# Kernel tuning notes

Hardware: AMD Instinct MI355X
Metric: run time of the kernel (lower is better)

Reference implementation:

```python
import jax, jax.numpy as jnp
import numpy as np

T, B, I, H = 512, 64, 512, 512


def setup_inputs() -> dict:
    key = jax.random.key(0)
    ks = jax.random.split(key, 24)
    s = (1.0 / H) ** 0.5  # uniform_(-sqrt(1/hidden), sqrt(1/hidden))
    u = lambda k, shape: jax.random.uniform(k, shape, jnp.float32, -s, s)
    inp = {
        "x": jax.random.normal(ks[0], (T, B, I), jnp.float32),
        "h0": u(ks[1], (B, H)),
        "c0": u(ks[2], (B, H)),
    }
    j = 3
    for g in ("ii", "if", "ig", "io"):
        inp["W_" + g] = u(ks[j], (I, H)); j += 1
        inp["b_" + g] = u(ks[j], (H,)); j += 1
    for g in ("hi", "hf", "hg", "ho"):
        inp["W_" + g] = u(ks[j], (H, H)); j += 1
        inp["b_" + g] = u(ks[j], (H,)); j += 1
    return inp


def reference(x, h0, c0, W_ii, b_ii, W_if, b_if, W_ig, b_ig, W_io, b_io,
              W_hi, b_hi, W_hf, b_hf, W_hg, b_hg, W_ho, b_ho):
    # Concatenating per-gate weights is mathematically identical to the 8
    # separate matmuls + bias adds in the source cell.
    Wx = jnp.concatenate([W_ii, W_if, W_ig, W_io], axis=1)        # [I, 4H]
    Wh = jnp.concatenate([W_hi, W_hf, W_hg, W_ho], axis=1)        # [H, 4H]
    b = jnp.concatenate([b_ii + b_hi, b_if + b_hf, b_ig + b_hg, b_io + b_ho])
    # Precompute all input projections in one big GEMM: [T, B, 4H]
    xg = jnp.einsum('tbi,ih->tbh', x, Wx) + b

    def step(carry, xg_t):
        h, c = carry
        gates = xg_t + h @ Wh                                      # [B, 4H]
        i_g, f_g, g_g, o_g = jnp.split(gates, 4, axis=-1)
        i = jax.nn.sigmoid(i_g)
        f = jax.nn.sigmoid(f_g)
        g = jnp.tanh(g_g)
        o = jax.nn.sigmoid(o_g)
        c1 = f * c + i * g
        h1 = o * c1  # NOTE: source applies o * c_1 WITHOUT tanh(c_1)
        return (h1, c1), h1

    (hT, cT), out = jax.lax.scan(step, (h0, c0), xg)               # out: [T, B, H]
    return (out, hT, cT)
```

## Files before the change

kernel.cpp:

```cpp
#include <hip/hip_runtime.h>
#include <stdint.h>


typedef __attribute__((ext_vector_type(8))) short    short8;
typedef __attribute__((ext_vector_type(4))) float    f32x4;
typedef __attribute__((ext_vector_type(4))) unsigned u32x4;
typedef __attribute__((ext_vector_type(2))) unsigned u32x2;

#define XG_OFF    0ull
#define WBT_OFF   134217728ull
#define BIAS_OFF  136314880ull
#define HW_OFF    136323072ull

static __device__ __forceinline__ unsigned short f2bf(float f) {
  unsigned u = __float_as_uint(f);
  unsigned r = (u + 0x7FFFu + ((u >> 16) & 1u)) >> 16;
  return (unsigned short)r;
}
static __device__ __forceinline__ float bf2f(unsigned short u) {
  return __uint_as_float(((unsigned)u) << 16);
}
static __device__ __forceinline__ float sigmoidf_(float x) {
  return 1.0f / (1.0f + __expf(-x));
}
static __device__ __forceinline__ float tanhf_(float x) {
  return 1.0f - 2.0f / (__expf(2.0f * x) + 1.0f);
}

__global__ void lstm_prep(const float* __restrict__ W_ii, const float* __restrict__ W_if,
                          const float* __restrict__ W_ig, const float* __restrict__ W_io,
                          const float* __restrict__ b_ii, const float* __restrict__ b_if,
                          const float* __restrict__ b_ig, const float* __restrict__ b_io,
                          const float* __restrict__ b_hi, const float* __restrict__ b_hf,
                          const float* __restrict__ b_hg, const float* __restrict__ b_ho,
                          const float* __restrict__ h0, unsigned char* ws)
{
  unsigned short*     WbT  = (unsigned short*)(ws + WBT_OFF);
  float*              bias = (float*)(ws + BIAS_OFF);
  unsigned long long* hw64 = (unsigned long long*)(ws + HW_OFF);

  const int gid = blockIdx.x * blockDim.x + threadIdx.x;
  const int gsz = gridDim.x * blockDim.x;

  for (int i = gid; i < 4 * 512 * 512; i += gsz) {
    int g = i >> 18, rem = i & 262143, c = rem >> 9, k = rem & 511;
    const float* W = (g == 0) ? W_ii : (g == 1) ? W_if : (g == 2) ? W_ig : W_io;
    WbT[(size_t)(g * 512 + c) * 512 + k] = f2bf(W[(size_t)k * 512 + c]);
  }
  for (int i = gid; i < 2048; i += gsz) {
    int g = i >> 9, c = i & 511;
    const float* bi = (g == 0) ? b_ii : (g == 1) ? b_if : (g == 2) ? b_ig : b_io;
    const float* bh = (g == 0) ? b_hi : (g == 1) ? b_hf : (g == 2) ? b_hg : b_ho;
    bias[i] = bi[c] + bh[c];
  }
  for (int i = gid; i < 64 * 256; i += gsz) {
    int r = i >> 8, wc = i & 255;
    int gb = r >> 4, row = r & 15, wsl = wc >> 6, c = wc & 63;
    unsigned lo = f2bf(h0[(size_t)r * 512 + wc * 2]);
    unsigned hi = f2bf(h0[(size_t)r * 512 + wc * 2 + 1]);
    hw64[((size_t)(gb * 4 + wsl) * 16 + row) * 64 + c] =
        (unsigned long long)(lo | (hi << 16));
  }
  for (int i = gid; i < 64 * 256; i += gsz)
    hw64[16384 + i] = 0xFFFFFFFF00000000ull;
}

__global__ __launch_bounds__(256) void xproj_gemm(const float* __restrict__ x,
                                                  unsigned char* ws)
{
  const unsigned short* WbT  = (const unsigned short*)(ws + WBT_OFF);
  const float*          bias = (const float*)(ws + BIAS_OFF);
  unsigned short*       xg   = (unsigned short*)(ws + XG_OFF);

  __shared__ unsigned short As[128 * 64];
  __shared__ unsigned short Bs[128 * 64];

  const int bid  = (int)blockIdx.x;
  const int bidx = (bid & 7) * 512 + (bid >> 3);
  const int bm = bidx >> 4, bn = bidx & 15;
  const int row0 = bm * 128, col0 = bn * 128;

  const int tid = threadIdx.x, lane = tid & 63, w = tid >> 6;
  const int wr = w >> 1, wc = w & 1;

  f32x4 acc[4][4] = {};

  for (int k0 = 0; k0 < 512; k0 += 64) {
    __syncthreads();
#pragma unroll
    for (int u = 0; u < 8; ++u) {
      int idx = u * 256 + tid;
      int r = idx >> 4, quad = idx & 15;
      const float4 v = *reinterpret_cast<const float4*>(
          &x[(size_t)(row0 + r) * 512 + k0 + quad * 4]);
      uint2 p;
      p.x = (unsigned)f2bf(v.x) | ((unsigned)f2bf(v.y) << 16);
      p.y = (unsigned)f2bf(v.z) | ((unsigned)f2bf(v.w) << 16);
      *reinterpret_cast<uint2*>(&As[r * 64 + quad * 4]) = p;
    }
#pragma unroll
    for (int u = 0; u < 4; ++u) {
      int idx = u * 256 + tid;
      int cl = idx >> 3, ch = idx & 7;
      *reinterpret_cast<uint4*>(&Bs[cl * 64 + ch * 8]) =
          *reinterpret_cast<const uint4*>(&WbT[(size_t)(col0 + cl) * 512 + k0 + ch * 8]);
    }
    __syncthreads();
#pragma unroll
    for (int kk = 0; kk < 64; kk += 32) {
      short8 a[4], b[4];
#pragma unroll
      for (int m = 0; m < 4; ++m)
        a[m] = *reinterpret_cast<const short8*>(
            &As[(wr * 64 + m * 16 + (lane & 15)) * 64 + kk + (lane >> 4) * 8]);
#pragma unroll
      for (int n = 0; n < 4; ++n)
        b[n] = *reinterpret_cast<const short8*>(
            &Bs[(wc * 64 + n * 16 + (lane & 15)) * 64 + kk + (lane >> 4) * 8]);
#pragma unroll
      for (int m = 0; m < 4; ++m)
#pragma unroll
        for (int n = 0; n < 4; ++n)
          acc[m][n] = __builtin_amdgcn_mfma_f32_16x16x32_bf16(a[m], b[n], acc[m][n], 0, 0, 0);
    }
  }
#pragma unroll
  for (int m = 0; m < 4; ++m) {
    int rowtile = bm * 8 + wr * 4 + m;
#pragma unroll
    for (int n = 0; n < 4; ++n) {
      int coltile = bn * 8 + wc * 4 + n;
      float bv = bias[coltile * 16 + (lane & 15)];
      uint2 p;
      p.x = (unsigned)f2bf(acc[m][n][0] + bv) | ((unsigned)f2bf(acc[m][n][1] + bv) << 16);
      p.y = (unsigned)f2bf(acc[m][n][2] + bv) | ((unsigned)f2bf(acc[m][n][3] + bv) << 16);
      *reinterpret_cast<uint2*>(&xg[((size_t)rowtile * 128 + coltile) * 256 + lane * 4]) = p;
    }
  }
}

__global__ __launch_bounds__(256, 1) void lstm_rec(
    const float* __restrict__ Whi, const float* __restrict__ Whf,
    const float* __restrict__ Whg, const float* __restrict__ Who,
    const float* __restrict__ c0, unsigned char* ws, float* __restrict__ out)
{
  const int gb = (int)blockIdx.x & 3;
  const int gc = (int)blockIdx.x >> 2;
  const int tid = threadIdx.x, lane = tid & 63, w = tid >> 6;

  const unsigned short* xg = (const unsigned short*)(ws + XG_OFF);
  unsigned long long*   hw64 = (unsigned long long*)(ws + HW_OFF);

  __shared__ unsigned hdat[4][1024];
  __shared__ float glds[2][4][4][16][16];

  short8 bhi[4][4], blo[4][4];
  {
    const int colg = gc * 16 + (lane & 15);
    const int krow = (lane >> 4) * 8;
#pragma unroll
    for (int g = 0; g < 4; ++g) {
      const float* P = (g == 0) ? Whi : (g == 1) ? Whf : (g == 2) ? Whg : Who;
#pragma unroll
      for (int kkl = 0; kkl < 4; ++kkl) {
        short8 h8, l8;
#pragma unroll
        for (int i = 0; i < 8; ++i) {
          int k = w * 128 + kkl * 32 + krow + i;
          float wv = P[(size_t)k * 512 + colg];
          unsigned short hb = f2bf(wv);
          h8[i] = (short)hb;
          l8[i] = (short)f2bf(wv - bf2f(hb));
        }
        bhi[g][kkl] = h8; blo[g][kkl] = l8;
      }
    }
  }

  const int crow = tid >> 4, ccol = tid & 15;
  float c = c0[(size_t)(gb * 16 + crow) * 512 + gc * 16 + ccol];

  float* hT = out + 16777216;
  float* cT = out + 16777216 + 32768;
  const int e_ix = (crow >> 2) * 64 + ccol * 4 + (crow & 3);
  int bleft = 30000000;

  for (int t = 0; t < 512; ++t) {
    const size_t xb = (size_t)(t * 4 + gb) * 128 * 256;
    float xgi = bf2f(xg[xb + (size_t)(0 * 32 + gc) * 256 + e_ix]);
    float xgf = bf2f(xg[xb + (size_t)(1 * 32 + gc) * 256 + e_ix]);
    float xgg = bf2f(xg[xb + (size_t)(2 * 32 + gc) * 256 + e_ix]);
    float xgo = bf2f(xg[xb + (size_t)(3 * 32 + gc) * 256 + e_ix]);

    const int par = t & 1;
    const unsigned long long* blk =
        hw64 + (size_t)((par * 4 + gb) * 4 + w) * 1024;
    const unsigned tagw = (unsigned)t;

    u32x4 dv[8];
    const char* lbase = (const char*)blk + lane * 16;
#pragma unroll
    for (int i = 0; i < 8; ++i)
      asm volatile("global_load_dwordx4 %0, %1, off sc0 sc1"
                   : "=v"(dv[i]) : "v"(lbase + (size_t)i * 1024));

    {
      const unsigned long long* pp =
          blk + (size_t)((lane & 3) * 4) * 64 + (lane >> 2) * 8;
      bool rdy;
      do {
        unsigned long long pv = 0;
        if (lane < 32)
          pv = __hip_atomic_load(pp, __ATOMIC_RELAXED, __HIP_MEMORY_SCOPE_AGENT);
        rdy = __all(lane >= 32 || (unsigned)(pv >> 32) == tagw);
      } while (!rdy && --bleft > 0);
    }

    bool ok;
    asm volatile("s_waitcnt vmcnt(0)"
                 : "+v"(dv[0]), "+v"(dv[1]), "+v"(dv[2]), "+v"(dv[3]),
                   "+v"(dv[4]), "+v"(dv[5]), "+v"(dv[6]), "+v"(dv[7])
                 :: "memory");
    ok = true;
#pragma unroll
    for (int i = 0; i < 8; ++i)
      ok = ok && (dv[i][1] == tagw) && (dv[i][3] == tagw);
    while (!__all(ok) && --bleft > 0) {
#pragma unroll
      for (int i = 0; i < 8; ++i)
        asm volatile("global_load_dwordx4 %0, %1, off sc0 sc1"
                     : "=v"(dv[i]) : "v"(lbase + (size_t)i * 1024));
      asm volatile("s_waitcnt vmcnt(0)"
                   : "+v"(dv[0]), "+v"(dv[1]), "+v"(dv[2]), "+v"(dv[3]),
                     "+v"(dv[4]), "+v"(dv[5]), "+v"(dv[6]), "+v"(dv[7])
                   :: "memory");
      ok = true;
#pragma unroll
      for (int i = 0; i < 8; ++i)
        ok = ok && (dv[i][1] == tagw) && (dv[i][3] == tagw);
    }

#pragma unroll
    for (int i = 0; i < 8; ++i) {
      int k = i * 128 + lane * 2;
      int row = k >> 6;
      int sw = k ^ ((row & 7) << 2);
      u32x2 p2; p2[0] = dv[i][0]; p2[1] = dv[i][2];
      *reinterpret_cast<u32x2*>(&hdat[w][sw]) = p2;
    }
    asm volatile("s_waitcnt lgkmcnt(0)" ::: "memory");
    __builtin_amdgcn_sched_barrier(0);

    f32x4 acc[4] = {};
#pragma unroll
    for (int kkl = 0; kkl < 4; ++kkl) {
      int base = (lane & 15) * 64 + kkl * 16 + (lane >> 4) * 4;
      int sw = base ^ ((lane & 7) << 2);
      union { u32x4 v; short8 s; } fr;
      fr.v = *reinterpret_cast<const u32x4*>(&hdat[w][sw]);
#pragma unroll
      for (int g = 0; g < 4; ++g) {
        acc[g] = __builtin_amdgcn_mfma_f32_16x16x32_bf16(fr.s, bhi[g][kkl], acc[g], 0, 0, 0);
        acc[g] = __builtin_amdgcn_mfma_f32_16x16x32_bf16(fr.s, blo[g][kkl], acc[g], 0, 0, 0);
      }
    }
#pragma unroll
    for (int g = 0; g < 4; ++g)
#pragma unroll
      for (int j = 0; j < 4; ++j)
        glds[par][w][g][(lane >> 4) * 4 + j][lane & 15] = acc[g][j];
    __syncthreads();

    float gi = xgi, gf = xgf, gg = xgg, go = xgo;
#pragma unroll
    for (int ww = 0; ww < 4; ++ww) {
      gi += glds[par][ww][0][crow][ccol];
      gf += glds[par][ww][1][crow][ccol];
      gg += glds[par][ww][2][crow][ccol];
      go += glds[par][ww][3][crow][ccol];
    }
    float iv = sigmoidf_(gi), fv = sigmoidf_(gf), gv = tanhf_(gg), ov = sigmoidf_(go);
    c = fv * c + iv * gv;
    float h = ov * c;

    if (t != 511) {
      float hp = __shfl_xor(h, 1);
      if ((ccol & 1) == 0) {
        unsigned data = (unsigned)f2bf(h) | ((unsigned)f2bf(hp) << 16);
        u32x2 wp; wp[0] = data; wp[1] = (unsigned)(t + 1);
        unsigned long long* dst =
            hw64 + ((size_t)((((t + 1) & 1) * 4 + gb) * 4 + (gc >> 3)) * 16 + crow) * 64 +
            (gc & 7) * 8 + (ccol >> 1);
        asm volatile("global_store_dwordx2 %0, %1, off sc0 sc1"
                     :: "v"(dst), "v"(wp) : "memory");
      }
    }

    out[(size_t)t * 32768 + (size_t)(gb * 16 + crow) * 512 + gc * 16 + ccol] = h;
    if (t == 511) {
      hT[(size_t)(gb * 16 + crow) * 512 + gc * 16 + ccol] = h;
      cT[(size_t)(gb * 16 + crow) * 512 + gc * 16 + ccol] = c;
    }
  }
}

extern "C" void kernel_launch(void* const* d_in, const int* in_sizes, int n_in,
                              void* d_out, int out_size, void* d_ws, size_t ws_size,
                              hipStream_t stream)
{
  const float* x    = (const float*)d_in[0];
  const float* h0   = (const float*)d_in[1];
  const float* c0   = (const float*)d_in[2];
  const float* W_ii = (const float*)d_in[3];
  const float* b_ii = (const float*)d_in[4];
  const float* W_if = (const float*)d_in[5];
  const float* b_if = (const float*)d_in[6];
  const float* W_ig = (const float*)d_in[7];
  const float* b_ig = (const float*)d_in[8];
  const float* W_io = (const float*)d_in[9];
  const float* b_io = (const float*)d_in[10];
  const float* W_hi = (const float*)d_in[11];
  const float* b_hi = (const float*)d_in[12];
  const float* W_hf = (const float*)d_in[13];
  const float* b_hf = (const float*)d_in[14];
  const float* W_hg = (const float*)d_in[15];
  const float* b_hg = (const float*)d_in[16];
  const float* W_ho = (const float*)d_in[17];
  const float* b_ho = (const float*)d_in[18];
  unsigned char* ws = (unsigned char*)d_ws;
  float* out = (float*)d_out;

  hipLaunchKernelGGL(lstm_prep, dim3(1024), dim3(256), 0, stream,
                     W_ii, W_if, W_ig, W_io, b_ii, b_if, b_ig, b_io,
                     b_hi, b_hf, b_hg, b_ho, h0, ws);
  hipLaunchKernelGGL(xproj_gemm, dim3(4096), dim3(256), 0, stream, x, ws);
  hipLaunchKernelGGL(lstm_rec, dim3(128), dim3(256), 0, stream,
                     W_hi, W_hf, W_hg, W_ho, c0, ws, out);
}
```

Before: 1.250 ms.

## Process two batch groups per recurrent block and halve the persistent grid

Each recurrent block now owns two 16-row batch groups for the same hidden column slice and processes them in turn each timestep, reusing the register-resident split-bf16 weights. The grid drops from 128 to 64 blocks, which shrinks the set of blocks taking part in the cross-block spin synchronization. The wait is also reordered: the h data is loaded optimistically and checked for the step tag first, and the flag poll runs only if that check fails. The cost is serial work per block per step, since the B group's wait and matmul happen after A's, which may lengthen each step's critical path.

```diff
diff --git a/kernel.cpp b/kernel.cpp
--- a/kernel.cpp
+++ b/kernel.cpp
@@ -144,8 +144,10 @@
     const float* __restrict__ Whg, const float* __restrict__ Who,
     const float* __restrict__ c0, unsigned char* ws, float* __restrict__ out)
 {
-  const int gb = (int)blockIdx.x & 3;
-  const int gc = (int)blockIdx.x >> 2;
+  const int bid = (int)blockIdx.x;
+  const int pr  = bid >> 5;
+  const int gc  = bid & 31;
+  const int gbA = pr * 2, gbB = pr * 2 + 1;
   const int tid = threadIdx.x, lane = tid & 63, w = tid >> 6;
 
   const unsigned short* xg = (const unsigned short*)(ws + XG_OFF);
@@ -178,7 +180,8 @@
   }
 
   const int crow = tid >> 4, ccol = tid & 15;
-  float c = c0[(size_t)(gb * 16 + crow) * 512 + gc * 16 + ccol];
+  float cA = c0[(size_t)(gbA * 16 + crow) * 512 + gc * 16 + ccol];
+  float cB = c0[(size_t)(gbB * 16 + crow) * 512 + gc * 16 + ccol];
 
   float* hT = out + 16777216;
   float* cT = out + 16777216 + 32768;
@@ -186,46 +189,26 @@
   int bleft = 30000000;
 
   for (int t = 0; t < 512; ++t) {
-    const size_t xb = (size_t)(t * 4 + gb) * 128 * 256;
-    float xgi = bf2f(xg[xb + (size_t)(0 * 32 + gc) * 256 + e_ix]);
-    float xgf = bf2f(xg[xb + (size_t)(1 * 32 + gc) * 256 + e_ix]);
-    float xgg = bf2f(xg[xb + (size_t)(2 * 32 + gc) * 256 + e_ix]);
-    float xgo = bf2f(xg[xb + (size_t)(3 * 32 + gc) * 256 + e_ix]);
-
     const int par = t & 1;
-    const unsigned long long* blk =
-        hw64 + (size_t)((par * 4 + gb) * 4 + w) * 1024;
     const unsigned tagw = (unsigned)t;
 
-    u32x4 dv[8];
-    const char* lbase = (const char*)blk + lane * 16;
-#pragma unroll
-    for (int i = 0; i < 8; ++i)
-      asm volatile("global_load_dwordx4 %0, %1, off sc0 sc1"
-                   : "=v"(dv[i]) : "v"(lbase + (size_t)i * 1024));
+    const size_t xbA = (size_t)(t * 4 + gbA) * 128 * 256;
+    const size_t xbB = (size_t)(t * 4 + gbB) * 128 * 256;
+    float xgiA = bf2f(xg[xbA + (size_t)(0 * 32 + gc) * 256 + e_ix]);
+    float xgfA = bf2f(xg[xbA + (size_t)(1 * 32 + gc) * 256 + e_ix]);
+    float xggA = bf2f(xg[xbA + (size_t)(2 * 32 + gc) * 256 + e_ix]);
+    float xgoA = bf2f(xg[xbA + (size_t)(3 * 32 + gc) * 256 + e_ix]);
+    float xgiB = bf2f(xg[xbB + (size_t)(0 * 32 + gc) * 256 + e_ix]);
+    float xgfB = bf2f(xg[xbB + (size_t)(1 * 32 + gc) * 256 + e_ix]);
+    float xggB = bf2f(xg[xbB + (size_t)(2 * 32 + gc) * 256 + e_ix]);
+    float xgoB = bf2f(xg[xbB + (size_t)(3 * 32 + gc) * 256 + e_ix]);
 
     {
-      const unsigned long long* pp =
-          blk + (size_t)((lane & 3) * 4) * 64 + (lane >> 2) * 8;
-      bool rdy;
-      do {
-        unsigned long long pv = 0;
-        if (lane < 32)
-          pv = __hip_atomic_load(pp, __ATOMIC_RELAXED, __HIP_MEMORY_SCOPE_AGENT);
-        rdy = __all(lane >= 32 || (unsigned)(pv >> 32) == tagw);
-      } while (!rdy && --bleft > 0);
-    }
-
-    bool ok;
-    asm volatile("s_waitcnt vmcnt(0)"
-                 : "+v"(dv[0]), "+v"(dv[1]), "+v"(dv[2]), "+v"(dv[3]),
-                   "+v"(dv[4]), "+v"(dv[5]), "+v"(dv[6]), "+v"(dv[7])
-                 :: "memory");
-    ok = true;
-#pragma unroll
-    for (int i = 0; i < 8; ++i)
-      ok = ok && (dv[i][1] == tagw) && (dv[i][3] == tagw);
-    while (!__all(ok) && --bleft > 0) {
+      const unsigned long long* blk =
+          hw64 + (size_t)((par * 4 + gbA) * 4 + w) * 1024;
+      const char* lbase = (const char*)blk + lane * 16;
+      u32x4 dv[8];
+      bool ok;
 #pragma unroll
       for (int i = 0; i < 8; ++i)
         asm volatile("global_load_dwordx4 %0, %1, off sc0 sc1"
@@ -238,68 +221,194 @@
 #pragma unroll
       for (int i = 0; i < 8; ++i)
         ok = ok && (dv[i][1] == tagw) && (dv[i][3] == tagw);
-    }
-
-#pragma unroll
-    for (int i = 0; i < 8; ++i) {
-      int k = i * 128 + lane * 2;
-      int row = k >> 6;
-      int sw = k ^ ((row & 7) << 2);
-      u32x2 p2; p2[0] = dv[i][0]; p2[1] = dv[i][2];
-      *reinterpret_cast<u32x2*>(&hdat[w][sw]) = p2;
-    }
-    asm volatile("s_waitcnt lgkmcnt(0)" ::: "memory");
-    __builtin_amdgcn_sched_barrier(0);
-
-    f32x4 acc[4] = {};
-#pragma unroll
-    for (int kkl = 0; kkl < 4; ++kkl) {
-      int base = (lane & 15) * 64 + kkl * 16 + (lane >> 4) * 4;
-      int sw = base ^ ((lane & 7) << 2);
-      union { u32x4 v; short8 s; } fr;
-      fr.v = *reinterpret_cast<const u32x4*>(&hdat[w][sw]);
-#pragma unroll
-      for (int g = 0; g < 4; ++g) {
-        acc[g] = __builtin_amdgcn_mfma_f32_16x16x32_bf16(fr.s, bhi[g][kkl], acc[g], 0, 0, 0);
-        acc[g] = __builtin_amdgcn_mfma_f32_16x16x32_bf16(fr.s, blo[g][kkl], acc[g], 0, 0, 0);
-      }
-    }
-#pragma unroll
-    for (int g = 0; g < 4; ++g)
-#pragma unroll
-      for (int j = 0; j < 4; ++j)
-        glds[par][w][g][(lane >> 4) * 4 + j][lane & 15] = acc[g][j];
-    __syncthreads();
-
-    float gi = xgi, gf = xgf, gg = xgg, go = xgo;
-#pragma unroll
-    for (int ww = 0; ww < 4; ++ww) {
-      gi += glds[par][ww][0][crow][ccol];
-      gf += glds[par][ww][1][crow][ccol];
-      gg += glds[par][ww][2][crow][ccol];
-      go += glds[par][ww][3][crow][ccol];
-    }
-    float iv = sigmoidf_(gi), fv = sigmoidf_(gf), gv = tanhf_(gg), ov = sigmoidf_(go);
-    c = fv * c + iv * gv;
-    float h = ov * c;
-
-    if (t != 511) {
-      float hp = __shfl_xor(h, 1);
-      if ((ccol & 1) == 0) {
-        unsigned data = (unsigned)f2bf(h) | ((unsigned)f2bf(hp) << 16);
-        u32x2 wp; wp[0] = data; wp[1] = (unsigned)(t + 1);
-        unsigned long long* dst =
-            hw64 + ((size_t)((((t + 1) & 1) * 4 + gb) * 4 + (gc >> 3)) * 16 + crow) * 64 +
-            (gc & 7) * 8 + (ccol >> 1);
-        asm volatile("global_store_dwordx2 %0, %1, off sc0 sc1"
-                     :: "v"(dst), "v"(wp) : "memory");
-      }
-    }
-
-    out[(size_t)t * 32768 + (size_t)(gb * 16 + crow) * 512 + gc * 16 + ccol] = h;
-    if (t == 511) {
-      hT[(size_t)(gb * 16 + crow) * 512 + gc * 16 + ccol] = h;
-      cT[(size_t)(gb * 16 + crow) * 512 + gc * 16 + ccol] = c;
+      if (!__all(ok)) {
+        const unsigned long long* pp =
+            blk + (size_t)((lane & 3) * 4) * 64 + (lane >> 2) * 8;
+        bool rdy;
+        do {
+          unsigned long long pv = 0;
+          if (lane < 32)
+            pv = __hip_atomic_load(pp, __ATOMIC_RELAXED, __HIP_MEMORY_SCOPE_AGENT);
+          rdy = __all(lane >= 32 || (unsigned)(pv >> 32) == tagw);
+        } while (!rdy && --bleft > 0);
+        do {
+#pragma unroll
+          for (int i = 0; i < 8; ++i)
+            asm volatile("global_load_dwordx4 %0, %1, off sc0 sc1"
+                         : "=v"(dv[i]) : "v"(lbase + (size_t)i * 1024));
+          asm volatile("s_waitcnt vmcnt(0)"
+                       : "+v"(dv[0]), "+v"(dv[1]), "+v"(dv[2]), "+v"(dv[3]),
+                         "+v"(dv[4]), "+v"(dv[5]), "+v"(dv[6]), "+v"(dv[7])
+                       :: "memory");
+          ok = true;
+#pragma unroll
+          for (int i = 0; i < 8; ++i)
+            ok = ok && (dv[i][1] == tagw) && (dv[i][3] == tagw);
+        } while (!__all(ok) && --bleft > 0);
+      }
+#pragma unroll
+      for (int i = 0; i < 8; ++i) {
+        int k = i * 128 + lane * 2;
+        int row = k >> 6;
+        int sw = k ^ ((row & 7) << 2);
+        u32x2 p2; p2[0] = dv[i][0]; p2[1] = dv[i][2];
+        *reinterpret_cast<u32x2*>(&hdat[w][sw]) = p2;
+      }
+      asm volatile("s_waitcnt lgkmcnt(0)" ::: "memory");
+      __builtin_amdgcn_sched_barrier(0);
+      f32x4 acc[4] = {};
+#pragma unroll
+      for (int kkl = 0; kkl < 4; ++kkl) {
+        int base = (lane & 15) * 64 + kkl * 16 + (lane >> 4) * 4;
+        int sw = base ^ ((lane & 7) << 2);
+        union { u32x4 v; short8 s; } fr;
+        fr.v = *reinterpret_cast<const u32x4*>(&hdat[w][sw]);
+#pragma unroll
+        for (int g = 0; g < 4; ++g) {
+          acc[g] = __builtin_amdgcn_mfma_f32_16x16x32_bf16(fr.s, bhi[g][kkl], acc[g], 0, 0, 0);
+          acc[g] = __builtin_amdgcn_mfma_f32_16x16x32_bf16(fr.s, blo[g][kkl], acc[g], 0, 0, 0);
+        }
+      }
+#pragma unroll
+      for (int g = 0; g < 4; ++g)
+#pragma unroll
+        for (int j = 0; j < 4; ++j)
+          glds[0][w][g][(lane >> 4) * 4 + j][lane & 15] = acc[g][j];
+      __syncthreads();
+
+      float gi = xgiA, gf = xgfA, gg = xggA, go = xgoA;
+#pragma unroll
+      for (int ww = 0; ww < 4; ++ww) {
+        gi += glds[0][ww][0][crow][ccol];
+        gf += glds[0][ww][1][crow][ccol];
+        gg += glds[0][ww][2][crow][ccol];
+        go += glds[0][ww][3][crow][ccol];
+      }
+      float iv = sigmoidf_(gi), fv = sigmoidf_(gf), gv = tanhf_(gg), ov = sigmoidf_(go);
+      cA = fv * cA + iv * gv;
+      float h = ov * cA;
+
+      if (t != 511) {
+        float hp = __shfl_xor(h, 1);
+        if ((ccol & 1) == 0) {
+          unsigned data = (unsigned)f2bf(h) | ((unsigned)f2bf(hp) << 16);
+          u32x2 wp; wp[0] = data; wp[1] = (unsigned)(t + 1);
+          unsigned long long* dst =
+              hw64 + ((size_t)((((t + 1) & 1) * 4 + gbA) * 4 + (gc >> 3)) * 16 + crow) * 64 +
+              (gc & 7) * 8 + (ccol >> 1);
+          asm volatile("global_store_dwordx2 %0, %1, off sc0 sc1"
+                       :: "v"(dst), "v"(wp) : "memory");
+        }
+      }
+      out[(size_t)t * 32768 + (size_t)(gbA * 16 + crow) * 512 + gc * 16 + ccol] = h;
+      if (t == 511) {
+        hT[(size_t)(gbA * 16 + crow) * 512 + gc * 16 + ccol] = h;
+        cT[(size_t)(gbA * 16 + crow) * 512 + gc * 16 + ccol] = cA;
+      }
+    }
+
+    {
+      const unsigned long long* blk =
+          hw64 + (size_t)((par * 4 + gbB) * 4 + w) * 1024;
+      const char* lbase = (const char*)blk + lane * 16;
+      u32x4 dv[8];
+      bool ok;
+#pragma unroll
+      for (int i = 0; i < 8; ++i)
+        asm volatile("global_load_dwordx4 %0, %1, off sc0 sc1"
+                     : "=v"(dv[i]) : "v"(lbase + (size_t)i * 1024));
+      asm volatile("s_waitcnt vmcnt(0)"
+                   : "+v"(dv[0]), "+v"(dv[1]), "+v"(dv[2]), "+v"(dv[3]),
+                     "+v"(dv[4]), "+v"(dv[5]), "+v"(dv[6]), "+v"(dv[7])
+                   :: "memory");
+      ok = true;
+#pragma unroll
+      for (int i = 0; i < 8; ++i)
+        ok = ok && (dv[i][1] == tagw) && (dv[i][3] == tagw);
+      if (!__all(ok)) {
+        const unsigned long long* pp =
+            blk + (size_t)((lane & 3) * 4) * 64 + (lane >> 2) * 8;
+        bool rdy;
+        do {
+          unsigned long long pv = 0;
+          if (lane < 32)
+            pv = __hip_atomic_load(pp, __ATOMIC_RELAXED, __HIP_MEMORY_SCOPE_AGENT);
+          rdy = __all(lane >= 32 || (unsigned)(pv >> 32) == tagw);
+        } while (!rdy && --bleft > 0);
+        do {
+#pragma unroll
+          for (int i = 0; i < 8; ++i)
+            asm volatile("global_load_dwordx4 %0, %1, off sc0 sc1"
+                         : "=v"(dv[i]) : "v"(lbase + (size_t)i * 1024));
+          asm volatile("s_waitcnt vmcnt(0)"
+                       : "+v"(dv[0]), "+v"(dv[1]), "+v"(dv[2]), "+v"(dv[3]),
+                         "+v"(dv[4]), "+v"(dv[5]), "+v"(dv[6]), "+v"(dv[7])
+                       :: "memory");
+          ok = true;
+#pragma unroll
+          for (int i = 0; i < 8; ++i)
+            ok = ok && (dv[i][1] == tagw) && (dv[i][3] == tagw);
+        } while (!__all(ok) && --bleft > 0);
+      }
+#pragma unroll
+      for (int i = 0; i < 8; ++i) {
+        int k = i * 128 + lane * 2;
+        int row = k >> 6;
+        int sw = k ^ ((row & 7) << 2);
+        u32x2 p2; p2[0] = dv[i][0]; p2[1] = dv[i][2];
+        *reinterpret_cast<u32x2*>(&hdat[w][sw]) = p2;
+      }
+      asm volatile("s_waitcnt lgkmcnt(0)" ::: "memory");
+      __builtin_amdgcn_sched_barrier(0);
+      f32x4 acc[4] = {};
+#pragma unroll
+      for (int kkl = 0; kkl < 4; ++kkl) {
+        int base = (lane & 15) * 64 + kkl * 16 + (lane >> 4) * 4;
+        int sw = base ^ ((lane & 7) << 2);
+        union { u32x4 v; short8 s; } fr;
+        fr.v = *reinterpret_cast<const u32x4*>(&hdat[w][sw]);
+#pragma unroll
+        for (int g = 0; g < 4; ++g) {
+          acc[g] = __builtin_amdgcn_mfma_f32_16x16x32_bf16(fr.s, bhi[g][kkl], acc[g], 0, 0, 0);
+          acc[g] = __builtin_amdgcn_mfma_f32_16x16x32_bf16(fr.s, blo[g][kkl], acc[g], 0, 0, 0);
+        }
+      }
+#pragma unroll
+      for (int g = 0; g < 4; ++g)
+#pragma unroll
+        for (int j = 0; j < 4; ++j)
+          glds[1][w][g][(lane >> 4) * 4 + j][lane & 15] = acc[g][j];
+      __syncthreads();
+
+      float gi = xgiB, gf = xgfB, gg = xggB, go = xgoB;
+#pragma unroll
+      for (int ww = 0; ww < 4; ++ww) {
+        gi += glds[1][ww][0][crow][ccol];
+        gf += glds[1][ww][1][crow][ccol];
+        gg += glds[1][ww][2][crow][ccol];
+        go += glds[1][ww][3][crow][ccol];
+      }
+      float iv = sigmoidf_(gi), fv = sigmoidf_(gf), gv = tanhf_(gg), ov = sigmoidf_(go);
+      cB = fv * cB + iv * gv;
+      float h = ov * cB;
+
+      if (t != 511) {
+        float hp = __shfl_xor(h, 1);
+        if ((ccol & 1) == 0) {
+          unsigned data = (unsigned)f2bf(h) | ((unsigned)f2bf(hp) << 16);
+          u32x2 wp; wp[0] = data; wp[1] = (unsigned)(t + 1);
+          unsigned long long* dst =
+              hw64 + ((size_t)((((t + 1) & 1) * 4 + gbB) * 4 + (gc >> 3)) * 16 + crow) * 64 +
+              (gc & 7) * 8 + (ccol >> 1);
+          asm volatile("global_store_dwordx2 %0, %1, off sc0 sc1"
+                       :: "v"(dst), "v"(wp) : "memory");
+        }
+      }
+      out[(size_t)t * 32768 + (size_t)(gbB * 16 + crow) * 512 + gc * 16 + ccol] = h;
+      if (t == 511) {
+        hT[(size_t)(gbB * 16 + crow) * 512 + gc * 16 + ccol] = h;
+        cT[(size_t)(gbB * 16 + crow) * 512 + gc * 16 + ccol] = cB;
+      }
     }
   }
 }
@@ -334,6 +443,6 @@
                      W_ii, W_if, W_ig, W_io, b_ii, b_if, b_ig, b_io,
                      b_hi, b_hf, b_hg, b_ho, h0, ws);
   hipLaunchKernelGGL(xproj_gemm, dim3(4096), dim3(256), 0, stream, x, ws);
-  hipLaunchKernelGGL(lstm_rec, dim3(128), dim3(256), 0, stream,
+  hipLaunchKernelGGL(lstm_rec, dim3(64), dim3(256), 0, stream,
                      W_hi, W_hf, W_hg, W_ho, c0, ws, out);
 }
```

Measured after the change: 2.041 ms. 63.3% more time.
